# Optimization experiments

Measured on AMD Instinct MI355X. Metric: run time of the kernel, lower is better.

## Reference

```python
import jax, jax.numpy as jnp
import numpy as np

B, C, CI, H, W = 8, 256, 128, 64, 64
EPS = 1e-5

def conv1x1(x, w, b):
    # x: [B,C,H,W], w: [O,C], b: [O]
    return jnp.einsum('bchw,oc->bohw', x, w) + b[None, :, None, None]

def avgpool2(x):
    b, c, h, w = x.shape
    return x.reshape(b, c, h // 2, 2, w // 2, 2).mean(axis=(3, 5))

def setup_inputs() -> dict:
    key = jax.random.key(0)
    ks = jax.random.split(key, 16)
    s = lambda fan: 1.0 / np.sqrt(fan)
    inp = {
        'q': jax.random.normal(ks[0], (B, C, H, W), jnp.float32),
        'k': jax.random.normal(ks[1], (B, C, H, W), jnp.float32),
        'v': jax.random.normal(ks[2], (B, C, H, W), jnp.float32),
        'Wg':  jax.random.normal(ks[3], (CI, C), jnp.float32) * s(C),
        'bg':  jax.random.normal(ks[4], (CI,), jnp.float32) * s(C),
        'Wth': jax.random.normal(ks[5], (CI, C), jnp.float32) * s(C),
        'bth': jax.random.normal(ks[6], (CI,), jnp.float32) * s(C),
        'Wph': jax.random.normal(ks[7], (CI, C), jnp.float32) * s(C),
        'bph': jax.random.normal(ks[8], (CI,), jnp.float32) * s(C),
        'Ww':  jax.random.normal(ks[9], (C, CI), jnp.float32) * s(CI),
        'bw':  jax.random.normal(ks[10], (C,), jnp.float32) * s(CI),
        'gamma': jax.random.normal(ks[11], (C,), jnp.float32) * 0.1 + 1.0,
        'beta':  jax.random.normal(ks[12], (C,), jnp.float32) * 0.1,
        'mean':  jax.random.normal(ks[13], (C,), jnp.float32) * 0.1,
        'var':   jax.random.uniform(ks[14], (C,), jnp.float32, 0.5, 1.5),
    }
    return inp

def reference(q, k, v, Wg, bg, Wth, bth, Wph, bph, Ww, bw, gamma, beta, mean, var):
    b = q.shape[0]
    # g branch on v, phi branch on q: 1x1 conv then 2x2 avg-pool (sub_sample)
    g_x = avgpool2(conv1x1(v, Wg, bg)).reshape(b, CI, -1)            # [B,CI,M]
    g_x = g_x.transpose(0, 2, 1)                                      # [B,M,CI]
    theta_x = conv1x1(k, Wth, bth).reshape(b, CI, -1).transpose(0, 2, 1)  # [B,N,CI]
    phi_x = avgpool2(conv1x1(q, Wph, bph)).reshape(b, CI, -1)        # [B,CI,M]
    f = jnp.einsum('bnc,bcm->bnm', theta_x, phi_x)                   # [B,N,M]
    f_div_C = jax.nn.softmax(f, axis=-1)
    y = jnp.einsum('bnm,bmc->bnc', f_div_C, g_x)                     # [B,N,CI]
    y = y.transpose(0, 2, 1).reshape(b, CI, H, W)
    W_y = conv1x1(y, Ww, bw)
    # BatchNorm2d (inference form)
    W_y = (W_y - mean[None, :, None, None]) * (gamma[None, :, None, None]
            * jax.lax.rsqrt(var + EPS)[None, :, None, None]) + beta[None, :, None, None]
    return W_y + v
```

## Files before the change

kernel.cpp:

```cpp
#include <hip/hip_runtime.h>
#include <cstddef>

typedef unsigned short u16;
typedef unsigned int u32;
typedef __attribute__((ext_vector_type(8))) __bf16 bf16x8;
typedef __attribute__((ext_vector_type(4))) float f32x4;

constexpr int kB = 8, kC = 256, kCI = 128, kN = 4096, kM = 1024;
constexpr float kEPS = 1e-5f;

__device__ __forceinline__ u16 f2bf(float f) {
    u32 u = __float_as_uint(f);
    u32 r = (u + 0x7fffu + ((u >> 16) & 1u)) >> 16;
    return (u16)r;
}

__global__ __launch_bounds__(256) void prep_kernel(const float* __restrict__ Wth,
                                                   const float* __restrict__ Wph,
                                                   const float* __restrict__ Wg,
                                                   const float* __restrict__ Ww,
                                                   const float* __restrict__ bw,
                                                   const float* __restrict__ gamma,
                                                   const float* __restrict__ beta,
                                                   const float* __restrict__ mean,
                                                   const float* __restrict__ var,
                                                   u16* __restrict__ Wthb,
                                                   u16* __restrict__ Wphb,
                                                   u16* __restrict__ Wgb,
                                                   u16* __restrict__ Wwsb,
                                                   float* __restrict__ bb) {
    int idx = blockIdx.x * 256 + threadIdx.x;
    if (idx < 32768) {
        Wthb[idx] = f2bf(Wth[idx]);
    } else if (idx < 65536) {
        int j = idx - 32768; Wphb[j] = f2bf(Wph[j]);
    } else if (idx < 98304) {
        int j = idx - 65536; Wgb[j] = f2bf(Wg[j]);
    } else {
        int j = idx - 98304;
        int co = j >> 7;
        float sc = gamma[co] * rsqrtf(var[co] + kEPS);
        Wwsb[j] = f2bf(Ww[j] * sc);
        if ((j & 127) == 0) bb[co] = (bw[co] - mean[co]) * sc + beta[co];
    }
}

template <int POOL>
__device__ __forceinline__ void conv_body(const float* __restrict__ x,
                                          const u16* __restrict__ Wb,
                                          const float* __restrict__ bias,
                                          u16* __restrict__ out, int Mn,
                                          int cmajor, int b, int n0) {
    __shared__ __align__(16) u16 w_lds[128 * 72];
    __shared__ __align__(16) u16 x_lds[64 * 64];
    int t = threadIdx.x;
    int w = t >> 6, lane = t & 63, l15 = lane & 15, quad = lane >> 4;
    int xn = t & 63, cbb = (t >> 6) * 2;

    f32x4 acc[8];
#pragma unroll
    for (int i = 0; i < 8; i++) acc[i] = (f32x4){0.f, 0.f, 0.f, 0.f};

    for (int c0 = 0; c0 < kC; c0 += 64) {
        __syncthreads();
#pragma unroll
        for (int i = 0; i < 4; i++) {
            int u = t + 256 * i;
            int ci = u >> 3, blk = u & 7;
            *(uint4*)&w_lds[ci * 72 + blk * 8] =
                *(const uint4*)&Wb[ci * kC + c0 + blk * 8];
        }
#pragma unroll
        for (int cc = 0; cc < 2; cc++) {
            int cb = cbb + cc;
            float f[8];
            if (POOL) {
                int p = n0 + xn, ph_ = p >> 5, pw_ = p & 31;
#pragma unroll
                for (int j = 0; j < 8; j++) {
                    const float* src = x + ((size_t)(b * kC + c0 + cb * 8 + j) * 64
                                            + 2 * ph_) * 64 + 2 * pw_;
                    float2 a = *(const float2*)src;
                    float2 b2 = *(const float2*)(src + 64);
                    f[j] = 0.25f * (a.x + a.y + b2.x + b2.y);
                }
            } else {
#pragma unroll
                for (int j = 0; j < 8; j++)
                    f[j] = x[(size_t)(b * kC + c0 + cb * 8 + j) * Mn + n0 + xn];
            }
            uint4 pk;
            pk.x = (u32)f2bf(f[0]) | ((u32)f2bf(f[1]) << 16);
            pk.y = (u32)f2bf(f[2]) | ((u32)f2bf(f[3]) << 16);
            pk.z = (u32)f2bf(f[4]) | ((u32)f2bf(f[5]) << 16);
            pk.w = (u32)f2bf(f[6]) | ((u32)f2bf(f[7]) << 16);
            *(uint4*)&x_lds[xn * 64 + ((cb ^ (xn & 7)) * 8)] = pk;
        }
        __syncthreads();

#pragma unroll
        for (int ks = 0; ks < 2; ks++) {
            int px = w * 16 + l15;
            bf16x8 xf = *(const bf16x8*)&x_lds[px * 64 + (((ks * 4 + quad) ^ (px & 7)) * 8)];
#pragma unroll
            for (int ct = 0; ct < 8; ct++) {
                bf16x8 wf = *(const bf16x8*)&w_lds[(ct * 16 + l15) * 72 + ks * 32 + quad * 8];
                if (cmajor)
                    acc[ct] = __builtin_amdgcn_mfma_f32_16x16x32_bf16(xf, wf, acc[ct], 0, 0, 0);
                else
                    acc[ct] = __builtin_amdgcn_mfma_f32_16x16x32_bf16(wf, xf, acc[ct], 0, 0, 0);
            }
        }
    }

    if (cmajor == 0) {
        int px = n0 + w * 16 + l15;
#pragma unroll
        for (int ct = 0; ct < 8; ct++) {
            int ci0 = ct * 16 + quad * 4;
            uint2 pk;
            pk.x = (u32)f2bf(acc[ct][0] + bias[ci0 + 0]) |
                   ((u32)f2bf(acc[ct][1] + bias[ci0 + 1]) << 16);
            pk.y = (u32)f2bf(acc[ct][2] + bias[ci0 + 2]) |
                   ((u32)f2bf(acc[ct][3] + bias[ci0 + 3]) << 16);
            *(uint2*)&out[(size_t)(b * Mn + px) * kCI + ci0] = pk;
        }
    } else {
        int px = n0 + w * 16 + quad * 4;
#pragma unroll
        for (int ct = 0; ct < 8; ct++) {
            int ci = ct * 16 + l15;
            float bs = bias[ci];
            uint2 pk;
            pk.x = (u32)f2bf(acc[ct][0] + bs) | ((u32)f2bf(acc[ct][1] + bs) << 16);
            pk.y = (u32)f2bf(acc[ct][2] + bs) | ((u32)f2bf(acc[ct][3] + bs) << 16);
            *(uint2*)&out[(size_t)(b * kCI + ci) * Mn + px] = pk;
        }
    }
}

__global__ __launch_bounds__(256) void convth_kernel(const float* __restrict__ x,
                                                     const u16* __restrict__ Wb,
                                                     const float* __restrict__ bias,
                                                     u16* __restrict__ out) {
    conv_body<0>(x, Wb, bias, out, kN, 0, blockIdx.y, blockIdx.x * 64);
}

__global__ __launch_bounds__(256) void convpg_kernel(const float* __restrict__ q,
                                                     const float* __restrict__ v,
                                                     const u16* __restrict__ Wph,
                                                     const u16* __restrict__ Wg,
                                                     const float* __restrict__ bph,
                                                     const float* __restrict__ bg,
                                                     u16* __restrict__ phi,
                                                     u16* __restrict__ g) {
    int z = blockIdx.z;
    conv_body<1>(z ? v : q, z ? Wg : Wph, z ? bg : bph, z ? g : phi,
                 kM, z, blockIdx.y, blockIdx.x * 64);
}

__global__ __launch_bounds__(256) void attn_kernel(const u16* __restrict__ theta,
                                                   const u16* __restrict__ phi,
                                                   const u16* __restrict__ g,
                                                   u16* __restrict__ y) {
    __shared__ __align__(16) u16 ph_lds[8192];
    __shared__ __align__(16) u16 g_lds[8192];
    __shared__ __align__(16) u16 p_lds[4096];

    int t = threadIdx.x, b = blockIdx.y, n0 = blockIdx.x * 64;
    int w = t >> 6, lane = t & 63, l15 = lane & 15, quad = lane >> 4;
    int sw = (l15 >> 1) & 3;

    bf16x8 thf[4];
    const u16* thB = theta + ((size_t)(b * kN) + n0 + w * 16 + l15) * kCI;
#pragma unroll
    for (int ks = 0; ks < 4; ks++)
        thf[ks] = *(const bf16x8*)&thB[ks * 32 + quad * 8];

    f32x4 oacc[8];
#pragma unroll
    for (int ct = 0; ct < 8; ct++) oacc[ct] = (f32x4){0.f, 0.f, 0.f, 0.f};
    float m_ = -1e30f, l_ = 0.f;

    const u16* phB = phi + (size_t)b * kM * kCI;
    const u16* gB  = g   + (size_t)b * kCI * kM;
    u16* pw = p_lds + w * 1024;

    for (int c0 = 0; c0 < kM; c0 += 64) {
        __syncthreads();
#pragma unroll
        for (int it = 0; it < 4; it++) {
            int u = t + 256 * it;
            int row = u >> 4, cb = u & 15;
            *(uint4*)&ph_lds[(cb >> 2) * 2048 + row * 32 + (((cb & 3) ^ ((row >> 1) & 3)) * 8)] =
                *(const uint4*)&phB[(size_t)(c0 + row) * kCI + cb * 8];
        }
#pragma unroll
        for (int it = 0; it < 4; it++) {
            int u = t + 256 * it;
            int ci = u >> 3, mb = u & 7;
            *(uint4*)&g_lds[(mb >> 2) * 4096 + ci * 32 + (((mb & 3) ^ ((ci >> 1) & 3)) * 8)] =
                *(const uint4*)&gB[(size_t)ci * kM + c0 + mb * 8];
        }
        __syncthreads();

        f32x4 sacc[4];
#pragma unroll
        for (int mt = 0; mt < 4; mt++) sacc[mt] = (f32x4){0.f, 0.f, 0.f, 0.f};
#pragma unroll
        for (int ks = 0; ks < 4; ks++)
#pragma unroll
            for (int mt = 0; mt < 4; mt++) {
                bf16x8 a = *(const bf16x8*)&ph_lds[ks * 2048 + (mt * 16 + l15) * 32 +
                                                   ((quad ^ sw) * 8)];
                sacc[mt] = __builtin_amdgcn_mfma_f32_16x16x32_bf16(a, thf[ks], sacc[mt], 0, 0, 0);
            }

        float mc = -1e30f;
#pragma unroll
        for (int mt = 0; mt < 4; mt++)
#pragma unroll
            for (int r = 0; r < 4; r++) mc = fmaxf(mc, sacc[mt][r]);
        mc = fmaxf(mc, __shfl_xor(mc, 16, 64));
        mc = fmaxf(mc, __shfl_xor(mc, 32, 64));
        float mn = fmaxf(m_, mc);
        int resc = __any(mn != m_);
        float alpha = __expf(m_ - mn);
        m_ = mn;
        float rs = 0.f;
#pragma unroll
        for (int mt = 0; mt < 4; mt++)
#pragma unroll
            for (int r = 0; r < 4; r++) {
                float p = __expf(sacc[mt][r] - mn);
                sacc[mt][r] = p;
                rs += p;
            }
        rs += __shfl_xor(rs, 16, 64);
        rs += __shfl_xor(rs, 32, 64);
        l_ = l_ * alpha + rs;
        if (resc) {
#pragma unroll
            for (int ct = 0; ct < 8; ct++)
#pragma unroll
                for (int r = 0; r < 4; r++) oacc[ct][r] *= alpha;
        }
#pragma unroll
        for (int mt = 0; mt < 4; mt++)
#pragma unroll
            for (int h = 0; h < 2; h++) {
                u32 d = (u32)f2bf(sacc[mt][2 * h]) | ((u32)f2bf(sacc[mt][2 * h + 1]) << 16);
                int m = mt * 16 + quad * 4 + 2 * h;
                int frag = m >> 5;
                int kblk = ((m >> 3) & 3);
                int j = (quad & 1) * 4 + 2 * h;
                *(u32*)&pw[frag * 512 + l15 * 32 + ((kblk ^ sw) * 8) + j] = d;
            }

#pragma unroll
        for (int ks2 = 0; ks2 < 2; ks2++) {
            bf16x8 bfrag = *(const bf16x8*)&pw[ks2 * 512 + l15 * 32 + ((quad ^ sw) * 8)];
#pragma unroll
            for (int ct = 0; ct < 8; ct++) {
                bf16x8 a = *(const bf16x8*)&g_lds[ks2 * 4096 + (ct * 16 + l15) * 32 +
                                                  ((quad ^ sw) * 8)];
                oacc[ct] = __builtin_amdgcn_mfma_f32_16x16x32_bf16(a, bfrag, oacc[ct], 0, 0, 0);
            }
        }
    }

    float inv = 1.0f / l_;
    int n = n0 + w * 16 + l15;
    u16* yr = y + ((size_t)(b * kN) + n) * kCI + quad * 4;
#pragma unroll
    for (int ct = 0; ct < 8; ct++) {
        uint2 pk;
        pk.x = (u32)f2bf(oacc[ct][0] * inv) | ((u32)f2bf(oacc[ct][1] * inv) << 16);
        pk.y = (u32)f2bf(oacc[ct][2] * inv) | ((u32)f2bf(oacc[ct][3] * inv) << 16);
        *(uint2*)&yr[ct * 16] = pk;
    }
}

__global__ __launch_bounds__(256) void final_kernel(const u16* __restrict__ y,
                                                    const u16* __restrict__ Wws,
                                                    const float* __restrict__ bb,
                                                    const float* __restrict__ v,
                                                    float* __restrict__ out) {
    __shared__ __align__(16) u16 y_lds[64 * 136];
    int t = threadIdx.x, b = blockIdx.y, n0 = blockIdx.x * 64;
    int w = t >> 6, lane = t & 63, l15 = lane & 15, quad = lane >> 4;

#pragma unroll
    for (int i = 0; i < 4; i++) {
        int u = t + 256 * i;
        int row = u >> 4, blk = u & 15;
        *(uint4*)&y_lds[row * 136 + blk * 8] =
            *(const uint4*)&y[(size_t)(b * kN + n0 + row) * kCI + blk * 8];
    }
    __syncthreads();

    bf16x8 af[4];
#pragma unroll
    for (int ks = 0; ks < 4; ks++)
        af[ks] = *(const bf16x8*)&y_lds[(w * 16 + l15) * 136 + ks * 32 + quad * 8];

#pragma unroll
    for (int ct = 0; ct < 16; ct++) {
        f32x4 a = (f32x4){0.f, 0.f, 0.f, 0.f};
#pragma unroll
        for (int ks = 0; ks < 4; ks++) {
            bf16x8 bf = *(const bf16x8*)&Wws[(ct * 16 + l15) * kCI + ks * 32 + quad * 8];
            a = __builtin_amdgcn_mfma_f32_16x16x32_bf16(af[ks], bf, a, 0, 0, 0);
        }
        int co = ct * 16 + l15;
        float bbv = bb[co];
        size_t base = (size_t)(b * kC + co) * kN + n0 + w * 16 + quad * 4;
        float4 vv = *(const float4*)&v[base];
        float4 ov;
        ov.x = a[0] + bbv + vv.x;
        ov.y = a[1] + bbv + vv.y;
        ov.z = a[2] + bbv + vv.z;
        ov.w = a[3] + bbv + vv.w;
        *(float4*)&out[base] = ov;
    }
}

extern "C" void kernel_launch(void* const* d_in, const int* in_sizes, int n_in,
                              void* d_out, int out_size, void* d_ws, size_t ws_size,
                              hipStream_t stream) {
    (void)in_sizes; (void)n_in; (void)out_size; (void)ws_size;
    const float* q     = (const float*)d_in[0];
    const float* k     = (const float*)d_in[1];
    const float* v     = (const float*)d_in[2];
    const float* Wg    = (const float*)d_in[3];
    const float* bg    = (const float*)d_in[4];
    const float* Wth   = (const float*)d_in[5];
    const float* bth   = (const float*)d_in[6];
    const float* Wph   = (const float*)d_in[7];
    const float* bph   = (const float*)d_in[8];
    const float* Ww    = (const float*)d_in[9];
    const float* bw    = (const float*)d_in[10];
    const float* gamma = (const float*)d_in[11];
    const float* beta  = (const float*)d_in[12];
    const float* mean  = (const float*)d_in[13];
    const float* var   = (const float*)d_in[14];
    float* out = (float*)d_out;

    u16* wsu = (u16*)d_ws;
    u16*   theta = wsu;
    u16*   phi   = theta + 4194304;
    u16*   gbuf  = phi + 1048576;
    u16*   ybuf  = gbuf + 1048576;
    u16*   Wthb  = ybuf + 4194304;
    u16*   Wphb  = Wthb + 32768;
    u16*   Wgb   = Wphb + 32768;
    u16*   Wwsb  = Wgb + 32768;
    float* bbuf  = (float*)(Wwsb + 32768);

    prep_kernel<<<dim3(512), 256, 0, stream>>>(Wth, Wph, Wg, Ww, bw, gamma, beta,
                                               mean, var, Wthb, Wphb, Wgb, Wwsb, bbuf);
    convth_kernel<<<dim3(64, 8), 256, 0, stream>>>(k, Wthb, bth, theta);
    convpg_kernel<<<dim3(16, 8, 2), 256, 0, stream>>>(q, v, Wphb, Wgb, bph, bg, phi, gbuf);
    attn_kernel<<<dim3(64, 8), 256, 0, stream>>>(theta, phi, gbuf, ybuf);
    final_kernel<<<dim3(64, 8), 256, 0, stream>>>(ybuf, Wwsb, bbuf, v, out);
}
```

Baseline: 256.0 us.

## Split attention over key dimension with partial outputs merged in final kernel

The attention kernel now splits the M (key) dimension into two halves across a third grid dimension, doubling the block count from 512 to 1024 for better CU occupancy. Each half writes fp32 partial outputs plus running max and sum, and the final kernel merges them before the output projection. The change also folds log2(e) into the theta weights and bias so the softmax can use exp2f, rescales only when the max grows by more than 8 (lazy rescaling), double-buffers phi tiles through registers, and reads g directly from global memory instead of staging it in LDS. In exchange it adds sizeable fp32 partial-output traffic to and from global memory.

```diff
diff --git a/kernel.cpp b/kernel.cpp
--- a/kernel.cpp
+++ b/kernel.cpp
@@ -7,7 +7,9 @@
 typedef __attribute__((ext_vector_type(4))) float f32x4;
 
 constexpr int kB = 8, kC = 256, kCI = 128, kN = 4096, kM = 1024;
+constexpr int kSPLIT = 2, kMCH = kM / kSPLIT, kNCH = kMCH / 64;
 constexpr float kEPS = 1e-5f;
+constexpr float kLOG2E = 1.44269504088896f;
 
 __device__ __forceinline__ u16 f2bf(float f) {
     u32 u = __float_as_uint(f);
@@ -16,6 +18,7 @@
 }
 
 __global__ __launch_bounds__(256) void prep_kernel(const float* __restrict__ Wth,
+                                                   const float* __restrict__ bth,
                                                    const float* __restrict__ Wph,
                                                    const float* __restrict__ Wg,
                                                    const float* __restrict__ Ww,
@@ -28,10 +31,12 @@
                                                    u16* __restrict__ Wphb,
                                                    u16* __restrict__ Wgb,
                                                    u16* __restrict__ Wwsb,
-                                                   float* __restrict__ bb) {
+                                                   float* __restrict__ bb,
+                                                   float* __restrict__ bthl) {
     int idx = blockIdx.x * 256 + threadIdx.x;
     if (idx < 32768) {
-        Wthb[idx] = f2bf(Wth[idx]);
+        Wthb[idx] = f2bf(Wth[idx] * kLOG2E);
+        if (idx < kCI) bthl[idx] = bth[idx] * kLOG2E;
     } else if (idx < 65536) {
         int j = idx - 32768; Wphb[j] = f2bf(Wph[j]);
     } else if (idx < 98304) {
@@ -159,15 +164,15 @@
                  kM, z, blockIdx.y, blockIdx.x * 64);
 }
 
-__global__ __launch_bounds__(256) void attn_kernel(const u16* __restrict__ theta,
-                                                   const u16* __restrict__ phi,
-                                                   const u16* __restrict__ g,
-                                                   u16* __restrict__ y) {
-    __shared__ __align__(16) u16 ph_lds[8192];
-    __shared__ __align__(16) u16 g_lds[8192];
+__global__ __launch_bounds__(256, 4) void attn_kernel(const u16* __restrict__ theta,
+                                                      const u16* __restrict__ phi,
+                                                      const u16* __restrict__ g,
+                                                      float* __restrict__ Opart,
+                                                      float* __restrict__ ml) {
+    __shared__ __align__(16) u16 ph_lds[16384];
     __shared__ __align__(16) u16 p_lds[4096];
 
-    int t = threadIdx.x, b = blockIdx.y, n0 = blockIdx.x * 64;
+    int t = threadIdx.x, b = blockIdx.y, n0 = blockIdx.x * 64, sp = blockIdx.z;
     int w = t >> 6, lane = t & 63, l15 = lane & 15, quad = lane >> 4;
     int sw = (l15 >> 1) & 3;
 
@@ -182,27 +187,32 @@
     for (int ct = 0; ct < 8; ct++) oacc[ct] = (f32x4){0.f, 0.f, 0.f, 0.f};
     float m_ = -1e30f, l_ = 0.f;
 
-    const u16* phB = phi + (size_t)b * kM * kCI;
-    const u16* gB  = g   + (size_t)b * kCI * kM;
+    const u16* phB = phi + ((size_t)b * kM + sp * kMCH) * kCI;
+    const u16* gB  = g + (size_t)b * kCI * kM + sp * kMCH;
     u16* pw = p_lds + w * 1024;
 
-    for (int c0 = 0; c0 < kM; c0 += 64) {
+    int ldo_[4], go_[4];
+#pragma unroll
+    for (int i = 0; i < 4; i++) {
+        int u = t + 256 * i, row = u >> 4, cb = u & 15;
+        ldo_[i] = (cb >> 2) * 2048 + row * 32 + (((cb & 3) ^ ((row >> 1) & 3)) * 8);
+        go_[i] = row * kCI + cb * 8;
+    }
+
+    uint4 preg[4];
+#pragma unroll
+    for (int i = 0; i < 4; i++) preg[i] = *(const uint4*)&phB[go_[i]];
+
+    for (int ch = 0; ch < kNCH; ch++) {
+        u16* buf = ph_lds + (ch & 1) * 8192;
+#pragma unroll
+        for (int i = 0; i < 4; i++) *(uint4*)&buf[ldo_[i]] = preg[i];
         __syncthreads();
-#pragma unroll
-        for (int it = 0; it < 4; it++) {
-            int u = t + 256 * it;
-            int row = u >> 4, cb = u & 15;
-            *(uint4*)&ph_lds[(cb >> 2) * 2048 + row * 32 + (((cb & 3) ^ ((row >> 1) & 3)) * 8)] =
-                *(const uint4*)&phB[(size_t)(c0 + row) * kCI + cb * 8];
-        }
-#pragma unroll
-        for (int it = 0; it < 4; it++) {
-            int u = t + 256 * it;
-            int ci = u >> 3, mb = u & 7;
-            *(uint4*)&g_lds[(mb >> 2) * 4096 + ci * 32 + (((mb & 3) ^ ((ci >> 1) & 3)) * 8)] =
-                *(const uint4*)&gB[(size_t)ci * kM + c0 + mb * 8];
-        }
-        __syncthreads();
+        if (ch + 1 < kNCH) {
+            const u16* nsrc = phB + (ch + 1) * 64 * kCI;
+#pragma unroll
+            for (int i = 0; i < 4; i++) preg[i] = *(const uint4*)&nsrc[go_[i]];
+        }
 
         f32x4 sacc[4];
 #pragma unroll
@@ -211,8 +221,8 @@
         for (int ks = 0; ks < 4; ks++)
 #pragma unroll
             for (int mt = 0; mt < 4; mt++) {
-                bf16x8 a = *(const bf16x8*)&ph_lds[ks * 2048 + (mt * 16 + l15) * 32 +
-                                                   ((quad ^ sw) * 8)];
+                bf16x8 a = *(const bf16x8*)&buf[ks * 2048 + (mt * 16 + l15) * 32 +
+                                                ((quad ^ sw) * 8)];
                 sacc[mt] = __builtin_amdgcn_mfma_f32_16x16x32_bf16(a, thf[ks], sacc[mt], 0, 0, 0);
             }
 
@@ -223,28 +233,29 @@
             for (int r = 0; r < 4; r++) mc = fmaxf(mc, sacc[mt][r]);
         mc = fmaxf(mc, __shfl_xor(mc, 16, 64));
         mc = fmaxf(mc, __shfl_xor(mc, 32, 64));
-        float mn = fmaxf(m_, mc);
-        int resc = __any(mn != m_);
-        float alpha = __expf(m_ - mn);
-        m_ = mn;
+        if (__any(mc > m_ + 8.0f)) {
+            float mn = fmaxf(m_, mc);
+            float al = exp2f(m_ - mn);
+            m_ = mn;
+            l_ *= al;
+#pragma unroll
+            for (int ct = 0; ct < 8; ct++)
+#pragma unroll
+                for (int r = 0; r < 4; r++) oacc[ct][r] *= al;
+        }
         float rs = 0.f;
 #pragma unroll
         for (int mt = 0; mt < 4; mt++)
 #pragma unroll
             for (int r = 0; r < 4; r++) {
-                float p = __expf(sacc[mt][r] - mn);
+                float p = exp2f(sacc[mt][r] - m_);
                 sacc[mt][r] = p;
                 rs += p;
             }
         rs += __shfl_xor(rs, 16, 64);
         rs += __shfl_xor(rs, 32, 64);
-        l_ = l_ * alpha + rs;
-        if (resc) {
-#pragma unroll
-            for (int ct = 0; ct < 8; ct++)
-#pragma unroll
-                for (int r = 0; r < 4; r++) oacc[ct][r] *= alpha;
-        }
+        l_ += rs;
+
 #pragma unroll
         for (int mt = 0; mt < 4; mt++)
 #pragma unroll
@@ -252,36 +263,39 @@
                 u32 d = (u32)f2bf(sacc[mt][2 * h]) | ((u32)f2bf(sacc[mt][2 * h + 1]) << 16);
                 int m = mt * 16 + quad * 4 + 2 * h;
                 int frag = m >> 5;
-                int kblk = ((m >> 3) & 3);
+                int kblk = (m >> 3) & 3;
                 int j = (quad & 1) * 4 + 2 * h;
                 *(u32*)&pw[frag * 512 + l15 * 32 + ((kblk ^ sw) * 8) + j] = d;
             }
 
+        const u16* gC = gB + ch * 64;
 #pragma unroll
         for (int ks2 = 0; ks2 < 2; ks2++) {
             bf16x8 bfrag = *(const bf16x8*)&pw[ks2 * 512 + l15 * 32 + ((quad ^ sw) * 8)];
 #pragma unroll
             for (int ct = 0; ct < 8; ct++) {
-                bf16x8 a = *(const bf16x8*)&g_lds[ks2 * 4096 + (ct * 16 + l15) * 32 +
-                                                  ((quad ^ sw) * 8)];
+                bf16x8 a = *(const bf16x8*)&gC[(size_t)(ct * 16 + l15) * kM +
+                                               ks2 * 32 + quad * 8];
                 oacc[ct] = __builtin_amdgcn_mfma_f32_16x16x32_bf16(a, bfrag, oacc[ct], 0, 0, 0);
             }
         }
     }
 
-    float inv = 1.0f / l_;
     int n = n0 + w * 16 + l15;
-    u16* yr = y + ((size_t)(b * kN) + n) * kCI + quad * 4;
-#pragma unroll
-    for (int ct = 0; ct < 8; ct++) {
-        uint2 pk;
-        pk.x = (u32)f2bf(oacc[ct][0] * inv) | ((u32)f2bf(oacc[ct][1] * inv) << 16);
-        pk.y = (u32)f2bf(oacc[ct][2] * inv) | ((u32)f2bf(oacc[ct][3] * inv) << 16);
-        *(uint2*)&yr[ct * 16] = pk;
-    }
-}
-
-__global__ __launch_bounds__(256) void final_kernel(const u16* __restrict__ y,
+    float* Ob = Opart + (((size_t)(sp * kB + b)) * kN + n) * kCI + quad * 4;
+#pragma unroll
+    for (int ct = 0; ct < 8; ct++)
+        *(f32x4*)&Ob[ct * 16] = oacc[ct];
+    if (quad == 0) {
+        float2 mv;
+        mv.x = m_;
+        mv.y = l_;
+        *(float2*)&ml[((size_t)(sp * kB + b) * kN + n) * 2] = mv;
+    }
+}
+
+__global__ __launch_bounds__(256) void final_kernel(const float* __restrict__ Opart,
+                                                    const float* __restrict__ ml,
                                                     const u16* __restrict__ Wws,
                                                     const float* __restrict__ bb,
                                                     const float* __restrict__ v,
@@ -290,12 +304,33 @@
     int t = threadIdx.x, b = blockIdx.y, n0 = blockIdx.x * 64;
     int w = t >> 6, lane = t & 63, l15 = lane & 15, quad = lane >> 4;
 
+    const float* O1 = Opart + (size_t)kB * kN * kCI;
 #pragma unroll
     for (int i = 0; i < 4; i++) {
-        int u = t + 256 * i;
-        int row = u >> 4, blk = u & 15;
-        *(uint4*)&y_lds[row * 136 + blk * 8] =
-            *(const uint4*)&y[(size_t)(b * kN + n0 + row) * kCI + blk * 8];
+        int u = t + 256 * i, row = u >> 4, c8 = u & 15;
+        int n = n0 + row;
+        size_t mi = (size_t)b * kN + n;
+        float2 ml0 = *(const float2*)&ml[mi * 2];
+        float2 ml1 = *(const float2*)&ml[(mi + (size_t)kB * kN) * 2];
+        float ms = fmaxf(ml0.x, ml1.x);
+        float w0 = exp2f(ml0.x - ms), w1 = exp2f(ml1.x - ms);
+        float inv = 1.0f / (ml0.y * w0 + ml1.y * w1);
+        float a0 = w0 * inv, a1 = w1 * inv;
+        size_t base = mi * kCI + c8 * 8;
+        float4 x0 = *(const float4*)&Opart[base];
+        float4 x0b = *(const float4*)&Opart[base + 4];
+        float4 x1 = *(const float4*)&O1[base];
+        float4 x1b = *(const float4*)&O1[base + 4];
+        uint4 pk;
+        pk.x = (u32)f2bf(x0.x * a0 + x1.x * a1) |
+               ((u32)f2bf(x0.y * a0 + x1.y * a1) << 16);
+        pk.y = (u32)f2bf(x0.z * a0 + x1.z * a1) |
+               ((u32)f2bf(x0.w * a0 + x1.w * a1) << 16);
+        pk.z = (u32)f2bf(x0b.x * a0 + x1b.x * a1) |
+               ((u32)f2bf(x0b.y * a0 + x1b.y * a1) << 16);
+        pk.w = (u32)f2bf(x0b.z * a0 + x1b.z * a1) |
+               ((u32)f2bf(x0b.w * a0 + x1b.w * a1) << 16);
+        *(uint4*)&y_lds[row * 136 + c8 * 8] = pk;
     }
     __syncthreads();
 
@@ -350,17 +385,20 @@
     u16*   theta = wsu;
     u16*   phi   = theta + 4194304;
     u16*   gbuf  = phi + 1048576;
-    u16*   ybuf  = gbuf + 1048576;
-    u16*   Wthb  = ybuf + 4194304;
+    u16*   Wthb  = gbuf + 1048576;
     u16*   Wphb  = Wthb + 32768;
     u16*   Wgb   = Wphb + 32768;
     u16*   Wwsb  = Wgb + 32768;
     float* bbuf  = (float*)(Wwsb + 32768);
-
-    prep_kernel<<<dim3(512), 256, 0, stream>>>(Wth, Wph, Wg, Ww, bw, gamma, beta,
-                                               mean, var, Wthb, Wphb, Wgb, Wwsb, bbuf);
-    convth_kernel<<<dim3(64, 8), 256, 0, stream>>>(k, Wthb, bth, theta);
+    float* bthl  = bbuf + 256;
+    float* mlb   = bthl + 128;
+    float* Opart = mlb + 2 * kB * kN * 2;
+
+    prep_kernel<<<dim3(512), 256, 0, stream>>>(Wth, bth, Wph, Wg, Ww, bw, gamma, beta,
+                                               mean, var, Wthb, Wphb, Wgb, Wwsb,
+                                               bbuf, bthl);
+    convth_kernel<<<dim3(64, 8), 256, 0, stream>>>(k, Wthb, bthl, theta);
     convpg_kernel<<<dim3(16, 8, 2), 256, 0, stream>>>(q, v, Wphb, Wgb, bph, bg, phi, gbuf);
-    attn_kernel<<<dim3(64, 8), 256, 0, stream>>>(theta, phi, gbuf, ybuf);
-    final_kernel<<<dim3(64, 8), 256, 0, stream>>>(ybuf, Wwsb, bbuf, v, out);
-}
+    attn_kernel<<<dim3(64, 8, 2), 256, 0, stream>>>(theta, phi, gbuf, Opart, mlb);
+    final_kernel<<<dim3(64, 8), 256, 0, stream>>>(Opart, mlb, Wwsb, bbuf, v, out);
+}
```

New measurement: 290.3 us. 13.4% more time.

## Split attention over key halves with 512 threads, exp2 softmax, lazy rescale

Applied to the files above, without the earlier changes.

The attention kernel now runs 512 threads per block, with each half of the waves processing half of the M keys. The two partial softmax states are merged through LDS at the end. Phi tiles are register-prefetched and G fragments are read directly from global memory instead of being staged in LDS. Theta weights and bias are prescaled by log2(e) so exp2f can be used, and the running-max rescale is skipped unless the max grows by more than 8. These changes aim to raise occupancy and parallelism and cut LDS traffic and exp cost. In exchange, G is read uncoalesced from global memory and unnormalised values can grow by up to about 2^8 before a rescale.

```diff
diff --git a/kernel.cpp b/kernel.cpp
--- a/kernel.cpp
+++ b/kernel.cpp
@@ -7,7 +7,9 @@
 typedef __attribute__((ext_vector_type(4))) float f32x4;
 
 constexpr int kB = 8, kC = 256, kCI = 128, kN = 4096, kM = 1024;
+constexpr int kHM = 512;
 constexpr float kEPS = 1e-5f;
+constexpr float kLOG2E = 1.44269504088896f;
 
 __device__ __forceinline__ u16 f2bf(float f) {
     u32 u = __float_as_uint(f);
@@ -16,6 +18,7 @@
 }
 
 __global__ __launch_bounds__(256) void prep_kernel(const float* __restrict__ Wth,
+                                                   const float* __restrict__ bth,
                                                    const float* __restrict__ Wph,
                                                    const float* __restrict__ Wg,
                                                    const float* __restrict__ Ww,
@@ -28,10 +31,12 @@
                                                    u16* __restrict__ Wphb,
                                                    u16* __restrict__ Wgb,
                                                    u16* __restrict__ Wwsb,
-                                                   float* __restrict__ bb) {
+                                                   float* __restrict__ bb,
+                                                   float* __restrict__ bthl) {
     int idx = blockIdx.x * 256 + threadIdx.x;
     if (idx < 32768) {
-        Wthb[idx] = f2bf(Wth[idx]);
+        Wthb[idx] = f2bf(Wth[idx] * kLOG2E);
+        if (idx < kCI) bthl[idx] = bth[idx] * kLOG2E;
     } else if (idx < 65536) {
         int j = idx - 32768; Wphb[j] = f2bf(Wph[j]);
     } else if (idx < 98304) {
@@ -159,20 +164,21 @@
                  kM, z, blockIdx.y, blockIdx.x * 64);
 }
 
-__global__ __launch_bounds__(256) void attn_kernel(const u16* __restrict__ theta,
-                                                   const u16* __restrict__ phi,
-                                                   const u16* __restrict__ g,
-                                                   u16* __restrict__ y) {
-    __shared__ __align__(16) u16 ph_lds[8192];
-    __shared__ __align__(16) u16 g_lds[8192];
-    __shared__ __align__(16) u16 p_lds[4096];
+__global__ __launch_bounds__(512, 4) void attn_kernel(const u16* __restrict__ theta,
+                                                      const u16* __restrict__ phi,
+                                                      const u16* __restrict__ g,
+                                                      u16* __restrict__ y) {
+    __shared__ __align__(16) u16 ph_lds[2][8192];
+    __shared__ __align__(16) u16 p_lds[8192];
+    __shared__ float mlsh[128];
 
     int t = threadIdx.x, b = blockIdx.y, n0 = blockIdx.x * 64;
     int w = t >> 6, lane = t & 63, l15 = lane & 15, quad = lane >> 4;
+    int half = w >> 2, wl = w & 3, th = t & 255;
     int sw = (l15 >> 1) & 3;
 
     bf16x8 thf[4];
-    const u16* thB = theta + ((size_t)(b * kN) + n0 + w * 16 + l15) * kCI;
+    const u16* thB = theta + ((size_t)(b * kN) + n0 + wl * 16 + l15) * kCI;
 #pragma unroll
     for (int ks = 0; ks < 4; ks++)
         thf[ks] = *(const bf16x8*)&thB[ks * 32 + quad * 8];
@@ -182,27 +188,33 @@
     for (int ct = 0; ct < 8; ct++) oacc[ct] = (f32x4){0.f, 0.f, 0.f, 0.f};
     float m_ = -1e30f, l_ = 0.f;
 
-    const u16* phB = phi + (size_t)b * kM * kCI;
-    const u16* gB  = g   + (size_t)b * kCI * kM;
+    const u16* phB = phi + ((size_t)b * kM + half * kHM) * kCI;
+    const u16* gB  = g + (size_t)b * kCI * kM + half * kHM;
+    u16* phh = ph_lds[half];
     u16* pw = p_lds + w * 1024;
 
-    for (int c0 = 0; c0 < kM; c0 += 64) {
+    int ldo_[4], go_[4];
+#pragma unroll
+    for (int i = 0; i < 4; i++) {
+        int u = th + 256 * i, row = u >> 4, cb = u & 15;
+        ldo_[i] = (cb >> 2) * 2048 + row * 32 + (((cb & 3) ^ ((row >> 1) & 3)) * 8);
+        go_[i] = row * kCI + cb * 8;
+    }
+
+    uint4 preg[4];
+#pragma unroll
+    for (int i = 0; i < 4; i++) preg[i] = *(const uint4*)&phB[go_[i]];
+
+    for (int ch = 0; ch < kHM / 64; ++ch) {
         __syncthreads();
 #pragma unroll
-        for (int it = 0; it < 4; it++) {
-            int u = t + 256 * it;
-            int row = u >> 4, cb = u & 15;
-            *(uint4*)&ph_lds[(cb >> 2) * 2048 + row * 32 + (((cb & 3) ^ ((row >> 1) & 3)) * 8)] =
-                *(const uint4*)&phB[(size_t)(c0 + row) * kCI + cb * 8];
-        }
-#pragma unroll
-        for (int it = 0; it < 4; it++) {
-            int u = t + 256 * it;
-            int ci = u >> 3, mb = u & 7;
-            *(uint4*)&g_lds[(mb >> 2) * 4096 + ci * 32 + (((mb & 3) ^ ((ci >> 1) & 3)) * 8)] =
-                *(const uint4*)&gB[(size_t)ci * kM + c0 + mb * 8];
-        }
+        for (int i = 0; i < 4; i++) *(uint4*)&phh[ldo_[i]] = preg[i];
         __syncthreads();
+        if (ch + 1 < kHM / 64) {
+            const u16* ns = phB + (ch + 1) * 64 * kCI;
+#pragma unroll
+            for (int i = 0; i < 4; i++) preg[i] = *(const uint4*)&ns[go_[i]];
+        }
 
         f32x4 sacc[4];
 #pragma unroll
@@ -211,8 +223,8 @@
         for (int ks = 0; ks < 4; ks++)
 #pragma unroll
             for (int mt = 0; mt < 4; mt++) {
-                bf16x8 a = *(const bf16x8*)&ph_lds[ks * 2048 + (mt * 16 + l15) * 32 +
-                                                   ((quad ^ sw) * 8)];
+                bf16x8 a = *(const bf16x8*)&phh[ks * 2048 + (mt * 16 + l15) * 32 +
+                                                ((quad ^ sw) * 8)];
                 sacc[mt] = __builtin_amdgcn_mfma_f32_16x16x32_bf16(a, thf[ks], sacc[mt], 0, 0, 0);
             }
 
@@ -223,28 +235,29 @@
             for (int r = 0; r < 4; r++) mc = fmaxf(mc, sacc[mt][r]);
         mc = fmaxf(mc, __shfl_xor(mc, 16, 64));
         mc = fmaxf(mc, __shfl_xor(mc, 32, 64));
-        float mn = fmaxf(m_, mc);
-        int resc = __any(mn != m_);
-        float alpha = __expf(m_ - mn);
-        m_ = mn;
+        if (__any(mc > m_ + 8.0f)) {
+            float mn = fmaxf(m_, mc);
+            float al = exp2f(m_ - mn);
+            m_ = mn;
+            l_ *= al;
+#pragma unroll
+            for (int ct = 0; ct < 8; ct++)
+#pragma unroll
+                for (int r = 0; r < 4; r++) oacc[ct][r] *= al;
+        }
         float rs = 0.f;
 #pragma unroll
         for (int mt = 0; mt < 4; mt++)
 #pragma unroll
             for (int r = 0; r < 4; r++) {
-                float p = __expf(sacc[mt][r] - mn);
+                float p = exp2f(sacc[mt][r] - m_);
                 sacc[mt][r] = p;
                 rs += p;
             }
         rs += __shfl_xor(rs, 16, 64);
         rs += __shfl_xor(rs, 32, 64);
-        l_ = l_ * alpha + rs;
-        if (resc) {
-#pragma unroll
-            for (int ct = 0; ct < 8; ct++)
-#pragma unroll
-                for (int r = 0; r < 4; r++) oacc[ct][r] *= alpha;
-        }
+        l_ += rs;
+
 #pragma unroll
         for (int mt = 0; mt < 4; mt++)
 #pragma unroll
@@ -252,32 +265,54 @@
                 u32 d = (u32)f2bf(sacc[mt][2 * h]) | ((u32)f2bf(sacc[mt][2 * h + 1]) << 16);
                 int m = mt * 16 + quad * 4 + 2 * h;
                 int frag = m >> 5;
-                int kblk = ((m >> 3) & 3);
+                int kblk = (m >> 3) & 3;
                 int j = (quad & 1) * 4 + 2 * h;
                 *(u32*)&pw[frag * 512 + l15 * 32 + ((kblk ^ sw) * 8) + j] = d;
             }
 
+        const u16* gC = gB + ch * 64;
 #pragma unroll
         for (int ks2 = 0; ks2 < 2; ks2++) {
             bf16x8 bfrag = *(const bf16x8*)&pw[ks2 * 512 + l15 * 32 + ((quad ^ sw) * 8)];
 #pragma unroll
             for (int ct = 0; ct < 8; ct++) {
-                bf16x8 a = *(const bf16x8*)&g_lds[ks2 * 4096 + (ct * 16 + l15) * 32 +
-                                                  ((quad ^ sw) * 8)];
+                bf16x8 a = *(const bf16x8*)&gC[(size_t)(ct * 16 + l15) * kM +
+                                               ks2 * 32 + quad * 8];
                 oacc[ct] = __builtin_amdgcn_mfma_f32_16x16x32_bf16(a, bfrag, oacc[ct], 0, 0, 0);
             }
         }
     }
 
-    float inv = 1.0f / l_;
-    int n = n0 + w * 16 + l15;
-    u16* yr = y + ((size_t)(b * kN) + n) * kCI + quad * 4;
-#pragma unroll
-    for (int ct = 0; ct < 8; ct++) {
-        uint2 pk;
-        pk.x = (u32)f2bf(oacc[ct][0] * inv) | ((u32)f2bf(oacc[ct][1] * inv) << 16);
-        pk.y = (u32)f2bf(oacc[ct][2] * inv) | ((u32)f2bf(oacc[ct][3] * inv) << 16);
-        *(uint2*)&yr[ct * 16] = pk;
+    __syncthreads();
+    float* olds = (float*)&ph_lds[0][0];
+    int nl = wl * 16 + l15;
+    if (half == 1) {
+#pragma unroll
+        for (int ct = 0; ct < 8; ct++) {
+            int s = (ct * 4 + quad) ^ (nl & 7);
+            *(f32x4*)&olds[nl * 128 + s * 4] = oacc[ct];
+        }
+        if (quad == 0) { mlsh[2 * nl] = m_; mlsh[2 * nl + 1] = l_; }
+    }
+    __syncthreads();
+    if (half == 0) {
+        float m1 = mlsh[2 * nl], l1 = mlsh[2 * nl + 1];
+        float mm = fmaxf(m_, m1);
+        float w0 = exp2f(m_ - mm), w1 = exp2f(m1 - mm);
+        float inv = 1.0f / (l_ * w0 + l1 * w1);
+        float a0 = w0 * inv, a1 = w1 * inv;
+        u16* yr = y + ((size_t)(b * kN) + n0 + nl) * kCI + quad * 4;
+#pragma unroll
+        for (int ct = 0; ct < 8; ct++) {
+            int s = (ct * 4 + quad) ^ (nl & 7);
+            f32x4 o1 = *(const f32x4*)&olds[nl * 128 + s * 4];
+            uint2 pk;
+            pk.x = (u32)f2bf(oacc[ct][0] * a0 + o1[0] * a1) |
+                   ((u32)f2bf(oacc[ct][1] * a0 + o1[1] * a1) << 16);
+            pk.y = (u32)f2bf(oacc[ct][2] * a0 + o1[2] * a1) |
+                   ((u32)f2bf(oacc[ct][3] * a0 + o1[3] * a1) << 16);
+            *(uint2*)&yr[ct * 16] = pk;
+        }
     }
 }
 
@@ -356,11 +391,13 @@
     u16*   Wgb   = Wphb + 32768;
     u16*   Wwsb  = Wgb + 32768;
     float* bbuf  = (float*)(Wwsb + 32768);
-
-    prep_kernel<<<dim3(512), 256, 0, stream>>>(Wth, Wph, Wg, Ww, bw, gamma, beta,
-                                               mean, var, Wthb, Wphb, Wgb, Wwsb, bbuf);
-    convth_kernel<<<dim3(64, 8), 256, 0, stream>>>(k, Wthb, bth, theta);
+    float* bthl  = bbuf + 256;
+
+    prep_kernel<<<dim3(512), 256, 0, stream>>>(Wth, bth, Wph, Wg, Ww, bw, gamma, beta,
+                                               mean, var, Wthb, Wphb, Wgb, Wwsb,
+                                               bbuf, bthl);
+    convth_kernel<<<dim3(64, 8), 256, 0, stream>>>(k, Wthb, bthl, theta);
     convpg_kernel<<<dim3(16, 8, 2), 256, 0, stream>>>(q, v, Wphb, Wgb, bph, bg, phi, gbuf);
-    attn_kernel<<<dim3(64, 8), 256, 0, stream>>>(theta, phi, gbuf, ybuf);
+    attn_kernel<<<dim3(64, 8), 512, 0, stream>>>(theta, phi, gbuf, ybuf);
     final_kernel<<<dim3(64, 8), 256, 0, stream>>>(ybuf, Wwsb, bbuf, v, out);
 }
```

Result: slower. 296.3 us (+15.8%).
